# Kernel tuning notes

Measured on AMD Instinct MI355X. Metric: run time of the kernel, lower is better.

## Reference

```python
import jax, jax.numpy as jnp
import numpy as np

B, S, D, H = 8, 1024, 512, 8
HD = D // H
NEG = -1000000000.0
LN_EPS = 1e-5


def setup_inputs() -> dict:
    key = jax.random.key(0)
    ks = jax.random.split(key, 16)
    sc = 0.02
    inp = {
        "query": jax.random.normal(ks[0], (B, S, D), jnp.float32),
        "inputs": jax.random.normal(ks[1], (B, S, D), jnp.float32),
        "ren_mat": jax.random.uniform(ks[2], (B, S, S), jnp.float32) * 5.0,
        "timestamp": jax.random.normal(ks[3], (B, S, S), jnp.float32),
        # causal mask: True where attention is disallowed (strictly upper triangular)
        "mask": jnp.triu(jnp.ones((1, S, S), jnp.bool_), k=1),
        "Wq": jax.random.normal(ks[4], (D, D), jnp.float32) * sc,
        "bq": jnp.zeros((D,), jnp.float32),
        "Wk": jax.random.normal(ks[5], (D, D), jnp.float32) * sc,
        "bk": jnp.zeros((D,), jnp.float32),
        "Wv": jax.random.normal(ks[6], (D, D), jnp.float32) * sc,
        "bv": jnp.zeros((D,), jnp.float32),
        "Wo": jax.random.normal(ks[7], (D, D), jnp.float32) * sc,
        "bo": jnp.zeros((D,), jnp.float32),
        "W1": jax.random.normal(ks[8], (D, D), jnp.float32) * sc,
        "b1": jnp.zeros((D,), jnp.float32),
        "ln_g": jnp.ones((D,), jnp.float32),
        "ln_b": jnp.zeros((D,), jnp.float32),
        "l1": jax.random.uniform(ks[9], (1,), jnp.float32),
    }
    return inp


def reference(query, inputs, ren_mat, timestamp, mask,
              Wq, bq, Wk, bk, Wv, bv, Wo, bo, W1, b1, ln_g, ln_b, l1):
    # QKV projections (qk_same=False path; q,k,v all computed from `inputs`)
    def proj(x, W, b):
        return (x @ W.T + b).reshape(B, S, H, HD).transpose(0, 2, 1, 3)  # (B,H,S,HD)

    q = proj(inputs, Wq, bq)
    k = proj(inputs, Wk, bk)
    v = proj(inputs, Wv, bv)

    m = mask[:, None]  # (1,1,S,S), broadcasts over batch & heads

    scores = jnp.einsum("bhqd,bhkd->bhqk", q, k) / jnp.sqrt(jnp.float32(HD))
    scores = jnp.where(m, NEG, scores)
    prob_attn = jax.nn.softmax(scores, axis=-1)

    # memory blend: log10(ren+1) and exp(-|t|), each masked, summed, softmaxed
    ren_feat = jnp.where(m, NEG, jnp.log10(ren_mat + 1.0)[:, None])      # (B,H,S,S)
    time_stamp = jnp.where(m, NEG, jnp.exp(-jnp.abs(timestamp))[:, None])
    mem_attn = jax.nn.softmax(ren_feat + time_stamp, axis=-1)

    l = l1  # (1,) learned blend coefficient
    prob_attn = (1.0 - l) * prob_attn + l * mem_attn

    out = jnp.einsum("bhqk,bhkd->bhqd", prob_attn, v)
    out = out.transpose(0, 2, 1, 3).reshape(B, S, D)
    out = out @ Wo.T + bo

    # residual FFN + layernorm (dropout disabled / eval mode)
    out = out + (out @ W1.T + b1)
    mu = jnp.mean(out, axis=-1, keepdims=True)
    var = jnp.var(out, axis=-1, keepdims=True)
    out = (out - mu) / jnp.sqrt(var + LN_EPS) * ln_g + ln_b
    return out
```

## Files before the change

### kernel.cpp

```cpp
#include <hip/hip_runtime.h>
#include <math.h>

constexpr int kB = 8, kS = 1024, kD = 512, kH = 8, kHD = 64;
constexpr int kM = kB * kS;

typedef __attribute__((ext_vector_type(8))) short s8v;
typedef __attribute__((ext_vector_type(4))) float f4v;
typedef __attribute__((ext_vector_type(4))) unsigned short u4v;

__device__ __forceinline__ unsigned short f2bf(float f) {
    union { float f; unsigned int u; } c; c.f = f;
    unsigned int u = c.u + 0x7FFFu + ((c.u >> 16) & 1u);
    return (unsigned short)(u >> 16);
}

__device__ __forceinline__ void gl2lds(const unsigned short* g, unsigned short* l) {
    __builtin_amdgcn_global_load_lds(
        (const __attribute__((address_space(1))) unsigned int*)g,
        (__attribute__((address_space(3))) unsigned int*)l, 16, 0, 0);
}

__global__ __launch_bounds__(256) void prep_kernel(
    const float* __restrict__ X, const float* __restrict__ Wq,
    const float* __restrict__ Wk, const float* __restrict__ Wv,
    const float* __restrict__ Wo, const float* __restrict__ W1,
    const float* __restrict__ ren, const float* __restrict__ ts,
    const float* __restrict__ bo_g,
    unsigned short* __restrict__ Xbf, unsigned short* __restrict__ Wqkv,
    unsigned short* __restrict__ WoT, unsigned short* __restrict__ W1bf,
    unsigned short* __restrict__ mem)
{
    __shared__ float red[4];
    const int t = threadIdx.x;
    if (blockIdx.x < 5120) {
        const int idx = blockIdx.x * 256 + t;
        const float* src; unsigned short* dst; int off; bool isw1 = false;
        if (idx < 1048576)      { src = X;  dst = Xbf;           off = idx; }
        else if (idx < 1114112) { src = Wq; dst = Wqkv;          off = idx - 1048576; }
        else if (idx < 1179648) { src = Wk; dst = Wqkv + 262144; off = idx - 1114112; }
        else if (idx < 1245184) { src = Wv; dst = Wqkv + 524288; off = idx - 1179648; }
        else                    { src = W1; dst = W1bf;          off = idx - 1245184; isw1 = true; }
        float4 v = ((const float4*)src)[off];
        if (isw1) {
            const int e0 = off * 4;
            const int row = e0 >> 9, col0 = e0 & 511;
            if (row >= col0 && row < col0 + 4) ((float*)&v)[row - col0] += 1.0f;
        }
        u4v p;
        p[0] = f2bf(v.x); p[1] = f2bf(v.y); p[2] = f2bf(v.z); p[3] = f2bf(v.w);
        ((u4v*)dst)[off] = p;
        return;
    }
    if (blockIdx.x >= 13312) {
        const int bi2 = blockIdx.x - 13312;
        if (bi2 < 64) {
            __shared__ float T[64][65];
            const int tr = bi2 >> 3, tc = bi2 & 7;
            const int rr0 = t >> 4, cc0 = (t & 15) * 4;
#pragma unroll
            for (int i2 = 0; i2 < 4; ++i2) {
                const int r = i2 * 16 + rr0;
                const float4 v = *(const float4*)&Wo[(size_t)(tr * 64 + r) * 512 + tc * 64 + cc0];
                T[r][cc0] = v.x; T[r][cc0 + 1] = v.y; T[r][cc0 + 2] = v.z; T[r][cc0 + 3] = v.w;
            }
            __syncthreads();
#pragma unroll
            for (int i2 = 0; i2 < 4; ++i2) {
                const int r2 = i2 * 16 + rr0;
                u4v p;
                p[0] = f2bf(T[cc0][r2]);     p[1] = f2bf(T[cc0 + 1][r2]);
                p[2] = f2bf(T[cc0 + 2][r2]); p[3] = f2bf(T[cc0 + 3][r2]);
                *(u4v*)&WoT[(size_t)(tc * 64 + r2) * 512 + tr * 64 + cc0] = p;
            }
        } else {
            WoT[262144 + t]       = f2bf(bo_g[t]);
            WoT[262144 + 256 + t] = f2bf(bo_g[t + 256]);
        }
        return;
    }
    const int bi = blockIdx.x - 5120;
    const int i = bi & (kS - 1);
    const float* renr = ren + (size_t)bi * kS;
    const float* tsr  = ts  + (size_t)bi * kS;
    unsigned short* memr = mem + (size_t)bi * kS;
    const int j0 = t * 4;
    float p4[4] = {0.0f, 0.0f, 0.0f, 0.0f};
    float lsum = 0.0f;
    if (j0 <= i) {
        const float4 r4 = *(const float4*)(renr + j0);
        const float4 t4 = *(const float4*)(tsr + j0);
        float rv[4] = {r4.x, r4.y, r4.z, r4.w};
        float tv[4] = {t4.x, t4.y, t4.z, t4.w};
#pragma unroll
        for (int e = 0; e < 4; ++e) {
            const int j = j0 + e;
            float p = 0.0f;
            if (j <= i) {
                const float val = 0.30102999566f * __log2f(rv[e] + 1.0f) + __expf(-fabsf(tv[e]));
                p = __expf(val);
            }
            p4[e] = p;
            lsum += p;
        }
    }
#pragma unroll
    for (int d = 1; d < 64; d <<= 1) lsum += __shfl_xor(lsum, d);
    if ((t & 63) == 0) red[t >> 6] = lsum;
    __syncthreads();
    const float Z = red[0] + red[1] + red[2] + red[3];
    const float inv = 1.0f / Z;
    u4v pk;
#pragma unroll
    for (int e = 0; e < 4; ++e) pk[e] = f2bf(p4[e] * inv);
    *(u4v*)(memr + j0) = pk;
}

template <int NT>
__device__ __forceinline__ void mfma_core2(
    const unsigned short* __restrict__ A, const unsigned short* __restrict__ B,
    int M0, int N0, unsigned short* As, unsigned short* Bs, f4v (&acc)[4][NT])
{
    const int t = threadIdx.x, w = t >> 6, lane = t & 63;
    const int l16 = lane & 15, quad = lane >> 4;
    const int wm = (w & 1) * 64, wn = (w >> 1) * (NT * 16);
    constexpr int NB = NT / 2;
    constexpr int ABUF = 128 * 32;
    constexpr int BBUF = NT * 32 * 32;

    const unsigned short* gA[2]; unsigned short* lA[2];
#pragma unroll
    for (int i = 0; i < 2; ++i) {
        const int r0 = w * 32 + i * 16;
        const int r = r0 + (lane >> 2);
        const int c = (lane & 3) ^ ((r >> 1) & 3);
        gA[i] = A + (size_t)(M0 + r) * 512 + c * 8;
        lA[i] = As + r0 * 32;
    }
    const unsigned short* gB[NB]; unsigned short* lB[NB];
#pragma unroll
    for (int i = 0; i < NB; ++i) {
        const int r0 = w * (16 * NB) + i * 16;
        const int r = r0 + (lane >> 2);
        const int c = (lane & 3) ^ ((r >> 1) & 3);
        gB[i] = B + (size_t)(N0 + r) * 512 + c * 8;
        lB[i] = Bs + r0 * 32;
    }

    const f4v zero = {0.0f, 0.0f, 0.0f, 0.0f};
#pragma unroll
    for (int mt = 0; mt < 4; ++mt)
#pragma unroll
        for (int nt = 0; nt < NT; ++nt) acc[mt][nt] = zero;

    gl2lds(gA[0], lA[0]);
    gl2lds(gA[1], lA[1]);
#pragma unroll
    for (int i = 0; i < NB; ++i) gl2lds(gB[i], lB[i]);

#pragma unroll 1
    for (int k0 = 0; k0 < 512; k0 += 32) {
        const int cur = (k0 >> 5) & 1;
        __syncthreads();
        if (k0 + 32 < 512) {
            const int nb = cur ^ 1;
            gl2lds(gA[0] + k0 + 32, lA[0] + nb * ABUF);
            gl2lds(gA[1] + k0 + 32, lA[1] + nb * ABUF);
#pragma unroll
            for (int i = 0; i < NB; ++i) gl2lds(gB[i] + k0 + 32, lB[i] + nb * BBUF);
        }
        s8v af[4], bf_[NT];
#pragma unroll
        for (int mt = 0; mt < 4; ++mt) {
            const int r = wm + mt * 16 + l16;
            const int p = r * 4 + (quad ^ ((r >> 1) & 3));
            af[mt] = *(const s8v*)&As[cur * ABUF + p * 8];
        }
#pragma unroll
        for (int nt = 0; nt < NT; ++nt) {
            const int r = wn + nt * 16 + l16;
            const int p = r * 4 + (quad ^ ((r >> 1) & 3));
            bf_[nt] = *(const s8v*)&Bs[cur * BBUF + p * 8];
        }
#pragma unroll
        for (int mt = 0; mt < 4; ++mt)
#pragma unroll
            for (int nt = 0; nt < NT; ++nt)
                acc[mt][nt] = __builtin_amdgcn_mfma_f32_16x16x32_bf16(
                    af[mt], bf_[nt], acc[mt][nt], 0, 0, 0);
    }
}

__global__ __launch_bounds__(256) void qkv_mfma_kernel(
    const unsigned short* __restrict__ Xbf, const unsigned short* __restrict__ Wqkv,
    const float* __restrict__ bq, const float* __restrict__ bk, const float* __restrict__ bv,
    const unsigned short* __restrict__ W1bf, const unsigned short* __restrict__ WoT,
    const float* __restrict__ b1,
    unsigned short* __restrict__ qbf, unsigned short* __restrict__ kbf,
    unsigned short* __restrict__ vTbf,
    unsigned short* __restrict__ Wcomb, float* __restrict__ bcomb)
{
    __shared__ __align__(16) unsigned short As[2 * 128 * 32];
    __shared__ __align__(16) unsigned short Bs[2 * 128 * 32];
    const int y = blockIdx.y;
    const int t = threadIdx.x, w = t >> 6, lane = t & 63;
    const int l16 = lane & 15, quad = lane >> 4;

    if (y == 12) {
        if (blockIdx.x >= 36) return;
        f4v acc[4][2];
        const int M0 = (blockIdx.x / 9) * 128, N0 = (blockIdx.x % 9) * 64;
        mfma_core2<2>(W1bf, WoT, M0, N0, As, Bs, acc);
        const int wm = (w & 1) * 64, wn = (w >> 1) * 32;
#pragma unroll
        for (int nt = 0; nt < 2; ++nt) {
            const int qq = N0 + wn + nt * 16 + l16;
#pragma unroll
            for (int mt = 0; mt < 4; ++mt)
#pragma unroll
                for (int rr = 0; rr < 4; ++rr) {
                    const int m = M0 + wm + mt * 16 + quad * 4 + rr;
                    if (qq < 512)       Wcomb[(size_t)m * 512 + qq] = f2bf(acc[mt][nt][rr]);
                    else if (qq == 512) bcomb[m] = acc[mt][nt][rr] + b1[m];
                }
        }
        return;
    }

    f4v acc[4][4];
    const int wm = (w & 1) * 64, wn = (w >> 1) * 64;
    if (y < 8) {
        const int M0 = blockIdx.x * 128, N0 = y * 128;
        mfma_core2<4>(Xbf, Wqkv, M0, N0, As, Bs, acc);
        const int z = N0 >> 9;
        const float* bias = (z == 0) ? bq : bk;
        unsigned short* out = (z == 0) ? qbf : kbf;
#pragma unroll
        for (int nt = 0; nt < 4; ++nt) {
            const int n512 = (N0 + wn + nt * 16 + l16) & 511;
            const int h = n512 >> 6, hd = n512 & 63;
            const float bv_ = bias[n512];
#pragma unroll
            for (int mt = 0; mt < 4; ++mt) {
#pragma unroll
                for (int rr = 0; rr < 4; ++rr) {
                    const int m = M0 + wm + mt * 16 + quad * 4 + rr;
                    const int b = m >> 10, s = m & (kS - 1);
                    out[(((size_t)b * kH + h) * kS + s) * kHD + hd] =
                        f2bf(acc[mt][nt][rr] + bv_);
                }
            }
        }
    } else {
        const int M0 = (y - 8) * 128, N0 = blockIdx.x * 128;
        mfma_core2<4>(Wqkv + (size_t)1024 * 512, Xbf, M0, N0, As, Bs, acc);
#pragma unroll
        for (int mt = 0; mt < 4; ++mt) {
#pragma unroll
            for (int rr = 0; rr < 4; ++rr) {
                const int vcol = M0 + wm + mt * 16 + quad * 4 + rr;
                const int h = vcol >> 6, hd = vcol & 63;
                const float bv_ = bv[vcol];
#pragma unroll
                for (int nt = 0; nt < 4; ++nt) {
                    const int sg = N0 + wn + nt * 16 + l16;
                    const int b = sg >> 10, s = sg & (kS - 1);
                    vTbf[(((size_t)b * kH + h) * kHD + hd) * kS + s] =
                        f2bf(acc[mt][nt][rr] + bv_);
                }
            }
        }
    }
}

__global__ __launch_bounds__(512, 2) void gemm_ln_kernel(
    const unsigned short* __restrict__ Abf, const unsigned short* __restrict__ Wcomb,
    const float* __restrict__ bcomb, const float* __restrict__ g,
    const float* __restrict__ bb, float* __restrict__ out)
{
    __shared__ __align__(16) unsigned short As[2 * 32 * 32];
    __shared__ __align__(16) unsigned short Bs[2 * 512 * 32];
    constexpr int ABUF = 32 * 32, BBUF = 512 * 32;
    const int t = threadIdx.x, w = t >> 6, lane = t & 63;
    const int l16 = lane & 15, quad = lane >> 4;
    const int M0 = blockIdx.x * 32;

    const unsigned short* gB[4]; unsigned short* lB[4];
#pragma unroll
    for (int i = 0; i < 4; ++i) {
        const int r0 = w * 64 + i * 16;
        const int r = r0 + (lane >> 2);
        const int c = (lane & 3) ^ ((r >> 1) & 3);
        gB[i] = Wcomb + (size_t)r * 512 + c * 8;
        lB[i] = Bs + r0 * 32;
    }
    const unsigned short* gA = nullptr; unsigned short* lA = nullptr;
    if (w < 2) {
        const int r0 = w * 16;
        const int r = r0 + (lane >> 2);
        const int c = (lane & 3) ^ ((r >> 1) & 3);
        gA = Abf + (size_t)(M0 + r) * 512 + c * 8;
        lA = As + r0 * 32;
    }

    const f4v zero = {0.0f, 0.0f, 0.0f, 0.0f};
    f4v acc[2][4];
#pragma unroll
    for (int mt = 0; mt < 2; ++mt)
#pragma unroll
        for (int nt = 0; nt < 4; ++nt) acc[mt][nt] = zero;

#pragma unroll
    for (int i = 0; i < 4; ++i) gl2lds(gB[i], lB[i]);
    if (w < 2) gl2lds(gA, lA);

#pragma unroll 1
    for (int k0 = 0; k0 < 512; k0 += 32) {
        const int cur = (k0 >> 5) & 1;
        __syncthreads();
        if (k0 + 32 < 512) {
            const int nb = cur ^ 1;
#pragma unroll
            for (int i = 0; i < 4; ++i) gl2lds(gB[i] + k0 + 32, lB[i] + nb * BBUF);
            if (w < 2) gl2lds(gA + k0 + 32, lA + nb * ABUF);
        }
        s8v af[2], bf_[4];
#pragma unroll
        for (int mt = 0; mt < 2; ++mt) {
            const int r = mt * 16 + l16;
            const int p = r * 4 + (quad ^ ((r >> 1) & 3));
            af[mt] = *(const s8v*)&As[cur * ABUF + p * 8];
        }
#pragma unroll
        for (int nt = 0; nt < 4; ++nt) {
            const int r = w * 64 + nt * 16 + l16;
            const int p = r * 4 + (quad ^ ((r >> 1) & 3));
            bf_[nt] = *(const s8v*)&Bs[cur * BBUF + p * 8];
        }
#pragma unroll
        for (int mt = 0; mt < 2; ++mt)
#pragma unroll
            for (int nt = 0; nt < 4; ++nt)
                acc[mt][nt] = __builtin_amdgcn_mfma_f32_16x16x32_bf16(
                    af[mt], bf_[nt], acc[mt][nt], 0, 0, 0);
    }

    float bias[4], gg[4], bbv[4];
#pragma unroll
    for (int nt = 0; nt < 4; ++nt) {
        const int n = w * 64 + nt * 16 + l16;
        bias[nt] = bcomb[n]; gg[nt] = g[n]; bbv[nt] = bb[n];
    }
#pragma unroll
    for (int mt = 0; mt < 2; ++mt)
#pragma unroll
        for (int nt = 0; nt < 4; ++nt)
#pragma unroll
            for (int rr = 0; rr < 4; ++rr) acc[mt][nt][rr] += bias[nt];

    float2* red = (float2*)Bs;
    float2* stats = (float2*)As;
#pragma unroll
    for (int mt = 0; mt < 2; ++mt)
#pragma unroll
        for (int rr = 0; rr < 4; ++rr) {
            float s = 0.0f, qq = 0.0f;
#pragma unroll
            for (int nt = 0; nt < 4; ++nt) {
                const float v = acc[mt][nt][rr];
                s += v; qq += v * v;
            }
            s += __shfl_xor(s, 1); qq += __shfl_xor(qq, 1);
            s += __shfl_xor(s, 2); qq += __shfl_xor(qq, 2);
            s += __shfl_xor(s, 4); qq += __shfl_xor(qq, 4);
            s += __shfl_xor(s, 8); qq += __shfl_xor(qq, 8);
            if (l16 == 0) red[w * 32 + mt * 16 + quad * 4 + rr] = make_float2(s, qq);
        }
    __syncthreads();
    if (t < 32) {
        float s = 0.0f, qq = 0.0f;
#pragma unroll
        for (int wv = 0; wv < 8; ++wv) {
            const float2 f2 = red[wv * 32 + t];
            s += f2.x; qq += f2.y;
        }
        const float mu = s * (1.0f / kD);
        const float var = qq * (1.0f / kD) - mu * mu;
        stats[t] = make_float2(mu, rsqrtf(var + 1e-5f));
    }
    __syncthreads();
#pragma unroll
    for (int mt = 0; mt < 2; ++mt)
#pragma unroll
        for (int rr = 0; rr < 4; ++rr) {
            const int row = mt * 16 + quad * 4 + rr;
            const float2 st = stats[row];
#pragma unroll
            for (int nt = 0; nt < 4; ++nt) {
                const int n = w * 64 + nt * 16 + l16;
                out[(size_t)(M0 + row) * kD + n] =
                    (acc[mt][nt][rr] - st.x) * st.y * gg[nt] + bbv[nt];
            }
        }
}

#define KFRAG(tile, r, c) (*(const s8v*)&(tile)[(size_t)(r) * 64 + ((((c) ^ ((r) & 7))) << 3)])
#define VFRAG(tile, r, c) (*(const s8v*)&(tile)[(size_t)(r) * 128 + ((((c) ^ ((r) & 15))) << 3)])

__global__ __launch_bounds__(256, 2) void flash_attn_kernel(
    const unsigned short* __restrict__ q, const unsigned short* __restrict__ k,
    const unsigned short* __restrict__ vT, const unsigned short* __restrict__ mem,
    const float* __restrict__ l1, unsigned short* __restrict__ aout)
{
    const int qp = blockIdx.x;
    const int hi = 15 - qp, lo = qp;
    const int h = blockIdx.y, b = blockIdx.z;
    const int bh = b * kH + h;
    const int t = threadIdx.x;
    const int w = t >> 6, lane = t & 63;
    const int quad = lane >> 4, l16 = lane & 15;
    const float lam = l1[0];

    __shared__ __align__(16) unsigned short KV[2][2][64 * 128];
    __shared__ __align__(16) unsigned short P_lds[4][16 * 128];

    const int tbase[2] = {hi * 64, lo * 64};
    s8v qa[2][2];
    const unsigned short* mbase[2];
#pragma unroll
    for (int ti = 0; ti < 2; ++ti) {
        const unsigned short* qrow = q + ((size_t)bh * kS + tbase[ti] + w * 16 + l16) * kHD;
        qa[ti][0] = *(const s8v*)(qrow + quad * 8);
        qa[ti][1] = *(const s8v*)(qrow + 32 + quad * 8);
        mbase[ti] = mem + ((size_t)b * kS + tbase[ti] + w * 16 + l16) * kS;
    }

    const unsigned short* kb = k + (size_t)bh * kS * kHD;
    const unsigned short* vb = vT + (size_t)bh * kHD * kS;

    const int nkt   = (hi >> 1) + 1;
    const int nktlo = (lo >> 1) + 1;

    const unsigned short* gsrc[8];
    int gstep[8];
    unsigned short* ldst[8];
#pragma unroll
    for (int u = 0; u < 8; ++u) {
        const int seg = w * 8 + u;
        if (seg < 16) {
            const int s = seg;
            const int rloc = s * 8 + (lane >> 3);
            const int chunk = (lane & 7) ^ ((lane >> 3) & 7);
            gsrc[u] = kb + (size_t)rloc * kHD + chunk * 8;
            gstep[u] = 128 * kHD;
            ldst[u] = &KV[0][0][s * 512];
        } else {
            const int s = seg - 16;
            const int d = s * 4 + (lane >> 4);
            const int chunk = (lane & 15) ^ ((lane >> 4) & 3) ^ ((s & 3) << 2);
            gsrc[u] = vb + (size_t)d * kS + chunk * 8;
            gstep[u] = 128;
            ldst[u] = &KV[0][1][s * 512];
        }
    }

#pragma unroll
    for (int u = 0; u < 8; ++u) gl2lds(gsrc[u], ldst[u]);

    const f4v zero = {0.0f, 0.0f, 0.0f, 0.0f};
    f4v Oa[2][4], Om[2][4];
    float lr[2][4];
#pragma unroll
    for (int ti = 0; ti < 2; ++ti)
#pragma unroll
        for (int nt = 0; nt < 4; ++nt) {
            Oa[ti][nt] = zero; Om[ti][nt] = zero; lr[ti][nt] = 0.0f;
        }

    for (int kt = 0; kt < nkt; ++kt) {
        __syncthreads();
        const int cur = kt & 1;
        if (kt + 1 < nkt) {
            const int boff = ((kt + 1) & 1) * 16384;
#pragma unroll
            for (int u = 0; u < 8; ++u)
                gl2lds(gsrc[u] + (size_t)(kt + 1) * gstep[u], ldst[u] + boff);
        }
        const bool alo = (kt < nktlo);
        s8v ma0[4], ma1[4];
#pragma unroll
        for (int ks = 0; ks < 4; ++ks)
            ma0[ks] = *(const s8v*)(mbase[0] + kt * 128 + ks * 32 + quad * 8);
        if (alo) {
#pragma unroll
            for (int ks = 0; ks < 4; ++ks)
                ma1[ks] = *(const s8v*)(mbase[1] + kt * 128 + ks * 32 + quad * 8);
        }
        const unsigned short* Kc = &KV[cur][0][0];
        const unsigned short* Vc = &KV[cur][1][0];

        s8v pa0[4], pa1[4];
        {
            const bool diag = (kt == nkt - 1);
#pragma unroll
            for (int ct = 0; ct < 8; ++ct) {
                const int r = ct * 16 + l16;
                const s8v kb0 = KFRAG(Kc, r, quad);
                const s8v kb1 = KFRAG(Kc, r, 4 + quad);
                f4v acc = zero;
                acc = __builtin_amdgcn_mfma_f32_16x16x32_bf16(qa[0][0], kb0, acc, 0, 0, 0);
                acc = __builtin_amdgcn_mfma_f32_16x16x32_bf16(qa[0][1], kb1, acc, 0, 0, 0);
#pragma unroll
                for (int rr = 0; rr < 4; ++rr) {
                    float p = __expf(acc[rr] * 0.125f);
                    if (diag && (kt * 128 + r) > (tbase[0] + w * 16 + quad * 4 + rr)) p = 0.0f;
                    lr[0][rr] += p;
                    const int pr = quad * 4 + rr;
                    const int ck = ct * 2 + (l16 >> 3);
                    P_lds[w][pr * 128 + (((ck ^ pr) & 15) << 3) + (l16 & 7)] = f2bf(p);
                }
            }
#pragma unroll
            for (int ks = 0; ks < 4; ++ks)
                pa0[ks] = *(const s8v*)&P_lds[w][l16 * 128 + ((((ks * 4 + quad) ^ l16) & 15) << 3)];
        }
        if (alo) {
            const bool diag = (kt == nktlo - 1);
#pragma unroll
            for (int ct = 0; ct < 8; ++ct) {
                const int r = ct * 16 + l16;
                const s8v kb0 = KFRAG(Kc, r, quad);
                const s8v kb1 = KFRAG(Kc, r, 4 + quad);
                f4v acc = zero;
                acc = __builtin_amdgcn_mfma_f32_16x16x32_bf16(qa[1][0], kb0, acc, 0, 0, 0);
                acc = __builtin_amdgcn_mfma_f32_16x16x32_bf16(qa[1][1], kb1, acc, 0, 0, 0);
#pragma unroll
                for (int rr = 0; rr < 4; ++rr) {
                    float p = __expf(acc[rr] * 0.125f);
                    if (diag && (kt * 128 + r) > (tbase[1] + w * 16 + quad * 4 + rr)) p = 0.0f;
                    lr[1][rr] += p;
                    const int pr = quad * 4 + rr;
                    const int ck = ct * 2 + (l16 >> 3);
                    P_lds[w][pr * 128 + (((ck ^ pr) & 15) << 3) + (l16 & 7)] = f2bf(p);
                }
            }
#pragma unroll
            for (int ks = 0; ks < 4; ++ks)
                pa1[ks] = *(const s8v*)&P_lds[w][l16 * 128 + ((((ks * 4 + quad) ^ l16) & 15) << 3)];
        }

#pragma unroll
        for (int nt = 0; nt < 4; ++nt) {
#pragma unroll
            for (int ks = 0; ks < 4; ++ks) {
                const s8v vfk = VFRAG(Vc, nt * 16 + l16, ks * 4 + quad);
                Oa[0][nt] = __builtin_amdgcn_mfma_f32_16x16x32_bf16(pa0[ks], vfk, Oa[0][nt], 0, 0, 0);
                Om[0][nt] = __builtin_amdgcn_mfma_f32_16x16x32_bf16(ma0[ks], vfk, Om[0][nt], 0, 0, 0);
                if (alo) {
                    Oa[1][nt] = __builtin_amdgcn_mfma_f32_16x16x32_bf16(pa1[ks], vfk, Oa[1][nt], 0, 0, 0);
                    Om[1][nt] = __builtin_amdgcn_mfma_f32_16x16x32_bf16(ma1[ks], vfk, Om[1][nt], 0, 0, 0);
                }
            }
        }
    }

#pragma unroll
    for (int ti = 0; ti < 2; ++ti) {
        float inv4[4];
#pragma unroll
        for (int rr = 0; rr < 4; ++rr) {
            float Z = lr[ti][rr];
            Z += __shfl_xor(Z, 1);
            Z += __shfl_xor(Z, 2);
            Z += __shfl_xor(Z, 4);
            Z += __shfl_xor(Z, 8);
            inv4[rr] = (1.0f - lam) / Z;
        }
        const int r0 = tbase[ti] + w * 16;
#pragma unroll
        for (int nt = 0; nt < 4; ++nt)
#pragma unroll
            for (int rr = 0; rr < 4; ++rr) {
                const int i = r0 + quad * 4 + rr;
                const int d = h * kHD + nt * 16 + l16;
                aout[((size_t)b * kS + i) * kD + d] =
                    f2bf(Oa[ti][nt][rr] * inv4[rr] + lam * Om[ti][nt][rr]);
            }
    }
}

extern "C" void kernel_launch(void* const* d_in, const int* in_sizes, int n_in,
                              void* d_out, int out_size, void* d_ws, size_t ws_size,
                              hipStream_t stream) {
    const float* X   = (const float*)d_in[1];
    const float* ren = (const float*)d_in[2];
    const float* ts  = (const float*)d_in[3];
    const float* Wq = (const float*)d_in[5];  const float* bq = (const float*)d_in[6];
    const float* Wk = (const float*)d_in[7];  const float* bk = (const float*)d_in[8];
    const float* Wv = (const float*)d_in[9];  const float* bv = (const float*)d_in[10];
    const float* Wo = (const float*)d_in[11]; const float* bo = (const float*)d_in[12];
    const float* W1 = (const float*)d_in[13]; const float* b1 = (const float*)d_in[14];
    const float* lng = (const float*)d_in[15]; const float* lnb = (const float*)d_in[16];
    const float* l1 = (const float*)d_in[17];
    float* out = (float*)d_out;

    char* wsb = (char*)d_ws;
    unsigned short* Xbf    = (unsigned short*)(wsb);
    unsigned short* Wqkvbf = (unsigned short*)(wsb + (8u  << 20));
    unsigned short* WoTbf  = (unsigned short*)(wsb + (10u << 20));
    unsigned short* W1bf   = (unsigned short*)(wsb + (11u << 20));
    unsigned short* qbf    = (unsigned short*)(wsb + (12u << 20));
    unsigned short* kbf    = (unsigned short*)(wsb + (20u << 20));
    unsigned short* vTbf   = (unsigned short*)(wsb + (28u << 20));
    unsigned short* membf  = (unsigned short*)(wsb + (36u << 20));
    unsigned short* aoutbf = (unsigned short*)(wsb + (52u << 20));
    unsigned short* Wcombf = (unsigned short*)(wsb + (60u << 20));
    float*          bcombf = (float*)        (wsb + (61u << 20));

    prep_kernel<<<dim3(13377), 256, 0, stream>>>(
        X, Wq, Wk, Wv, Wo, W1, ren, ts, bo, Xbf, Wqkvbf, WoTbf, W1bf, membf);
    qkv_mfma_kernel<<<dim3(kM / 128, 13), 256, 0, stream>>>(
        Xbf, Wqkvbf, bq, bk, bv, W1bf, WoTbf, b1, qbf, kbf, vTbf, Wcombf, bcombf);
    flash_attn_kernel<<<dim3(8, kH, kB), 256, 0, stream>>>(
        qbf, kbf, vTbf, membf, l1, aoutbf);
    gemm_ln_kernel<<<dim3(kM / 32), 512, 0, stream>>>(
        aoutbf, Wcombf, bcombf, lng, lnb, out);
}
```

Before: 287.7 us.

## Split paired query tiles into one tile per attention block, heavy-first order

```diff
diff --git a/kernel.cpp b/kernel.cpp
--- a/kernel.cpp
+++ b/kernel.cpp
@@ -411,10 +411,9 @@
     const unsigned short* __restrict__ vT, const unsigned short* __restrict__ mem,
     const float* __restrict__ l1, unsigned short* __restrict__ aout)
 {
-    const int qp = blockIdx.x;
-    const int hi = 15 - qp, lo = qp;
-    const int h = blockIdx.y, b = blockIdx.z;
-    const int bh = b * kH + h;
+    const int bh = blockIdx.x;
+    const int qt = 15 - blockIdx.y;
+    const int b = bh >> 3, h = bh & 7;
     const int t = threadIdx.x;
     const int w = t >> 6, lane = t & 63;
     const int quad = lane >> 4, l16 = lane & 15;
@@ -423,22 +422,16 @@
     __shared__ __align__(16) unsigned short KV[2][2][64 * 128];
     __shared__ __align__(16) unsigned short P_lds[4][16 * 128];
 
-    const int tbase[2] = {hi * 64, lo * 64};
-    s8v qa[2][2];
-    const unsigned short* mbase[2];
-#pragma unroll
-    for (int ti = 0; ti < 2; ++ti) {
-        const unsigned short* qrow = q + ((size_t)bh * kS + tbase[ti] + w * 16 + l16) * kHD;
-        qa[ti][0] = *(const s8v*)(qrow + quad * 8);
-        qa[ti][1] = *(const s8v*)(qrow + 32 + quad * 8);
-        mbase[ti] = mem + ((size_t)b * kS + tbase[ti] + w * 16 + l16) * kS;
-    }
+    const int qbase = qt * 64;
+    const unsigned short* qrow = q + ((size_t)bh * kS + qbase + w * 16 + l16) * kHD;
+    const s8v qa0 = *(const s8v*)(qrow + quad * 8);
+    const s8v qa1 = *(const s8v*)(qrow + 32 + quad * 8);
+    const unsigned short* mbase = mem + ((size_t)b * kS + qbase + w * 16 + l16) * kS;
 
     const unsigned short* kb = k + (size_t)bh * kS * kHD;
     const unsigned short* vb = vT + (size_t)bh * kHD * kS;
 
-    const int nkt   = (hi >> 1) + 1;
-    const int nktlo = (lo >> 1) + 1;
+    const int nkt = (qt >> 1) + 1;
 
     const unsigned short* gsrc[8];
     int gstep[8];
@@ -467,14 +460,10 @@
     for (int u = 0; u < 8; ++u) gl2lds(gsrc[u], ldst[u]);
 
     const f4v zero = {0.0f, 0.0f, 0.0f, 0.0f};
-    f4v Oa[2][4], Om[2][4];
-    float lr[2][4];
-#pragma unroll
-    for (int ti = 0; ti < 2; ++ti)
-#pragma unroll
-        for (int nt = 0; nt < 4; ++nt) {
-            Oa[ti][nt] = zero; Om[ti][nt] = zero; lr[ti][nt] = 0.0f;
-        }
+    f4v Oa[4], Om[4];
+    float lr[4];
+#pragma unroll
+    for (int nt = 0; nt < 4; ++nt) { Oa[nt] = zero; Om[nt] = zero; lr[nt] = 0.0f; }
 
     for (int kt = 0; kt < nkt; ++kt) {
         __syncthreads();
@@ -485,107 +474,68 @@
             for (int u = 0; u < 8; ++u)
                 gl2lds(gsrc[u] + (size_t)(kt + 1) * gstep[u], ldst[u] + boff);
         }
-        const bool alo = (kt < nktlo);
-        s8v ma0[4], ma1[4];
+        s8v ma[4];
 #pragma unroll
         for (int ks = 0; ks < 4; ++ks)
-            ma0[ks] = *(const s8v*)(mbase[0] + kt * 128 + ks * 32 + quad * 8);
-        if (alo) {
-#pragma unroll
-            for (int ks = 0; ks < 4; ++ks)
-                ma1[ks] = *(const s8v*)(mbase[1] + kt * 128 + ks * 32 + quad * 8);
-        }
+            ma[ks] = *(const s8v*)(mbase + kt * 128 + ks * 32 + quad * 8);
+
         const unsigned short* Kc = &KV[cur][0][0];
         const unsigned short* Vc = &KV[cur][1][0];
-
-        s8v pa0[4], pa1[4];
-        {
-            const bool diag = (kt == nkt - 1);
-#pragma unroll
-            for (int ct = 0; ct < 8; ++ct) {
-                const int r = ct * 16 + l16;
-                const s8v kb0 = KFRAG(Kc, r, quad);
-                const s8v kb1 = KFRAG(Kc, r, 4 + quad);
-                f4v acc = zero;
-                acc = __builtin_amdgcn_mfma_f32_16x16x32_bf16(qa[0][0], kb0, acc, 0, 0, 0);
-                acc = __builtin_amdgcn_mfma_f32_16x16x32_bf16(qa[0][1], kb1, acc, 0, 0, 0);
-#pragma unroll
-                for (int rr = 0; rr < 4; ++rr) {
-                    float p = __expf(acc[rr] * 0.125f);
-                    if (diag && (kt * 128 + r) > (tbase[0] + w * 16 + quad * 4 + rr)) p = 0.0f;
-                    lr[0][rr] += p;
-                    const int pr = quad * 4 + rr;
-                    const int ck = ct * 2 + (l16 >> 3);
-                    P_lds[w][pr * 128 + (((ck ^ pr) & 15) << 3) + (l16 & 7)] = f2bf(p);
-                }
-            }
-#pragma unroll
-            for (int ks = 0; ks < 4; ++ks)
-                pa0[ks] = *(const s8v*)&P_lds[w][l16 * 128 + ((((ks * 4 + quad) ^ l16) & 15) << 3)];
-        }
-        if (alo) {
-            const bool diag = (kt == nktlo - 1);
-#pragma unroll
-            for (int ct = 0; ct < 8; ++ct) {
-                const int r = ct * 16 + l16;
-                const s8v kb0 = KFRAG(Kc, r, quad);
-                const s8v kb1 = KFRAG(Kc, r, 4 + quad);
-                f4v acc = zero;
-                acc = __builtin_amdgcn_mfma_f32_16x16x32_bf16(qa[1][0], kb0, acc, 0, 0, 0);
-                acc = __builtin_amdgcn_mfma_f32_16x16x32_bf16(qa[1][1], kb1, acc, 0, 0, 0);
-#pragma unroll
-                for (int rr = 0; rr < 4; ++rr) {
-                    float p = __expf(acc[rr] * 0.125f);
-                    if (diag && (kt * 128 + r) > (tbase[1] + w * 16 + quad * 4 + rr)) p = 0.0f;
-                    lr[1][rr] += p;
-                    const int pr = quad * 4 + rr;
-                    const int ck = ct * 2 + (l16 >> 3);
-                    P_lds[w][pr * 128 + (((ck ^ pr) & 15) << 3) + (l16 & 7)] = f2bf(p);
-                }
-            }
-#pragma unroll
-            for (int ks = 0; ks < 4; ++ks)
-                pa1[ks] = *(const s8v*)&P_lds[w][l16 * 128 + ((((ks * 4 + quad) ^ l16) & 15) << 3)];
-        }
-
+        const bool last = (kt == nkt - 1);
+
+#pragma unroll
+        for (int ct = 0; ct < 8; ++ct) {
+            const int r = ct * 16 + l16;
+            const s8v kb0 = KFRAG(Kc, r, quad);
+            const s8v kb1 = KFRAG(Kc, r, 4 + quad);
+            f4v acc = zero;
+            acc = __builtin_amdgcn_mfma_f32_16x16x32_bf16(qa0, kb0, acc, 0, 0, 0);
+            acc = __builtin_amdgcn_mfma_f32_16x16x32_bf16(qa1, kb1, acc, 0, 0, 0);
+#pragma unroll
+            for (int rr = 0; rr < 4; ++rr) {
+                float p = __expf(acc[rr] * 0.125f);
+                if (last && (kt * 128 + r) > (qbase + w * 16 + quad * 4 + rr)) p = 0.0f;
+                lr[rr] += p;
+                const int pr = quad * 4 + rr;
+                const int ck = ct * 2 + (l16 >> 3);
+                P_lds[w][pr * 128 + (((ck ^ pr) & 15) << 3) + (l16 & 7)] = f2bf(p);
+            }
+        }
+        s8v pa[4];
+#pragma unroll
+        for (int ks = 0; ks < 4; ++ks)
+            pa[ks] = *(const s8v*)&P_lds[w][l16 * 128 + ((((ks * 4 + quad) ^ l16) & 15) << 3)];
 #pragma unroll
         for (int nt = 0; nt < 4; ++nt) {
 #pragma unroll
             for (int ks = 0; ks < 4; ++ks) {
                 const s8v vfk = VFRAG(Vc, nt * 16 + l16, ks * 4 + quad);
-                Oa[0][nt] = __builtin_amdgcn_mfma_f32_16x16x32_bf16(pa0[ks], vfk, Oa[0][nt], 0, 0, 0);
-                Om[0][nt] = __builtin_amdgcn_mfma_f32_16x16x32_bf16(ma0[ks], vfk, Om[0][nt], 0, 0, 0);
-                if (alo) {
-                    Oa[1][nt] = __builtin_amdgcn_mfma_f32_16x16x32_bf16(pa1[ks], vfk, Oa[1][nt], 0, 0, 0);
-                    Om[1][nt] = __builtin_amdgcn_mfma_f32_16x16x32_bf16(ma1[ks], vfk, Om[1][nt], 0, 0, 0);
-                }
-            }
-        }
-    }
-
-#pragma unroll
-    for (int ti = 0; ti < 2; ++ti) {
-        float inv4[4];
+                Oa[nt] = __builtin_amdgcn_mfma_f32_16x16x32_bf16(pa[ks], vfk, Oa[nt], 0, 0, 0);
+                Om[nt] = __builtin_amdgcn_mfma_f32_16x16x32_bf16(ma[ks], vfk, Om[nt], 0, 0, 0);
+            }
+        }
+    }
+
+    float inv4[4];
+#pragma unroll
+    for (int rr = 0; rr < 4; ++rr) {
+        float Z = lr[rr];
+        Z += __shfl_xor(Z, 1);
+        Z += __shfl_xor(Z, 2);
+        Z += __shfl_xor(Z, 4);
+        Z += __shfl_xor(Z, 8);
+        inv4[rr] = (1.0f - lam) / Z;
+    }
+    const int r0 = qbase + w * 16;
+#pragma unroll
+    for (int nt = 0; nt < 4; ++nt)
 #pragma unroll
         for (int rr = 0; rr < 4; ++rr) {
-            float Z = lr[ti][rr];
-            Z += __shfl_xor(Z, 1);
-            Z += __shfl_xor(Z, 2);
-            Z += __shfl_xor(Z, 4);
-            Z += __shfl_xor(Z, 8);
-            inv4[rr] = (1.0f - lam) / Z;
-        }
-        const int r0 = tbase[ti] + w * 16;
-#pragma unroll
-        for (int nt = 0; nt < 4; ++nt)
-#pragma unroll
-            for (int rr = 0; rr < 4; ++rr) {
-                const int i = r0 + quad * 4 + rr;
-                const int d = h * kHD + nt * 16 + l16;
-                aout[((size_t)b * kS + i) * kD + d] =
-                    f2bf(Oa[ti][nt][rr] * inv4[rr] + lam * Om[ti][nt][rr]);
-            }
-    }
+            const int i = r0 + quad * 4 + rr;
+            const int d = h * kHD + nt * 16 + l16;
+            aout[((size_t)b * kS + i) * kD + d] =
+                f2bf(Oa[nt][rr] * inv4[rr] + lam * Om[nt][rr]);
+        }
 }
 
 extern "C" void kernel_launch(void* const* d_in, const int* in_sizes, int n_in,
@@ -620,7 +570,7 @@
         X, Wq, Wk, Wv, Wo, W1, ren, ts, bo, Xbf, Wqkvbf, WoTbf, W1bf, membf);
     qkv_mfma_kernel<<<dim3(kM / 128, 13), 256, 0, stream>>>(
         Xbf, Wqkvbf, bq, bk, bv, W1bf, WoTbf, b1, qbf, kbf, vTbf, Wcombf, bcombf);
-    flash_attn_kernel<<<dim3(8, kH, kB), 256, 0, stream>>>(
+    flash_attn_kernel<<<dim3(64, 16), 256, 0, stream>>>(
         qbf, kbf, vTbf, membf, l1, aoutbf);
     gemm_ln_kernel<<<dim3(kM / 32), 512, 0, stream>>>(
         aoutbf, Wcombf, bcombf, lng, lnb, out);
```

Measured after the change: 236.1 us. 1.22x faster.
